# Optimization experiments

Measured on AMD Instinct MI355X. Metric: run time of the kernel, lower is better.

## Reference

```python
import jax, jax.numpy as jnp
import numpy as np

B, C, H, W = 8, 256, 56, 56
K = 3  # kernel size


def _unfold3x3(x):
    """torch nn.Unfold(kernel=3, stride=1, pad=1) -> [B, HW, C*9].

    torch orders the unfolded channel dim as (c, ki, kj) with c slowest.
    """
    b, c, h, w = x.shape
    xp = jnp.pad(x, ((0, 0), (0, 0), (1, 1), (1, 1)))
    # stack 9 shifted views -> [B, C, 9, H, W]
    patches = jnp.stack(
        [xp[:, :, i:i + h, j:j + w] for i in range(K) for j in range(K)],
        axis=2,
    )
    return patches.reshape(b, c * K * K, h * w).transpose(0, 2, 1)


def setup_inputs() -> dict:
    key = jax.random.key(0)
    ks = jax.random.split(key, 8)
    d = C * K * K  # 2304
    s1 = 1.0 / np.sqrt(d)
    s2 = 1.0 / np.sqrt(C)
    return {
        "x": jax.random.normal(ks[0], (B, C, H, W), jnp.float32),
        "W1": jax.random.uniform(ks[1], (d, C), jnp.float32, -s1, s1),
        "b1": jax.random.uniform(ks[2], (C,), jnp.float32, -s1, s1),
        "W2": jax.random.uniform(ks[3], (C, d), jnp.float32, -s2, s2),
        "b2": jax.random.uniform(ks[4], (d,), jnp.float32, -s2, s2),
        "W3": jax.random.uniform(ks[5], (d, C), jnp.float32, -s1, s1),
        "b3": jax.random.uniform(ks[6], (C,), jnp.float32, -s1, s1),
    }


def reference(x, W1, b1, W2, b2, W3, b3):
    t = _unfold3x3(x)                                   # [B, HW, C*9]
    h1 = jax.nn.relu(jnp.einsum('bld,dc->blc', t, W1) + b1)   # [B, HW, C]
    s = jax.nn.sigmoid(jnp.einsum('blc,cd->bld', h1, W2) + b2)  # [B, HW, C*9]
    out = jnp.einsum('bld,dc->blc', t * s, W3) + b3     # [B, HW, C]
    return out
```

## Files before the change

kernel.cpp:

```cpp
#include <hip/hip_runtime.h>

typedef unsigned short u16;
typedef unsigned int u32;
typedef __attribute__((ext_vector_type(8))) short bfrag_t;
typedef __attribute__((ext_vector_type(4))) float accfrag_t;

__device__ __forceinline__ u16 f2b(float f) {
    u32 u = __float_as_uint(f);
    u32 r = (u + 0x7FFFu + ((u >> 16) & 1u)) >> 16;
    return (u16)r;
}
__device__ __forceinline__ float b2f(u16 b) {
    return __uint_as_float(((u32)b) << 16);
}

__device__ __forceinline__ void load16(const u16* g, u16* l) {
    __builtin_amdgcn_global_load_lds(
        (__attribute__((address_space(1))) void*)(u16*)g,
        (__attribute__((address_space(3))) void*)l,
        16, 0, 0);
}

__global__ __launch_bounds__(256) void k_xtp(const float* __restrict__ x,
                                             u16* __restrict__ xtp) {
    const int bh = blockIdx.x;
    const int b = bh / 58;
    const int hp = bh - b * 58;
    const int tid = threadIdx.x;
    u16* rowbase = xtp + (size_t)(b * 58 + hp) * 58 * 256;
    if (hp == 0 || hp == 57) {
        u32* p = (u32*)rowbase;
        for (int i = tid; i < 58 * 128; i += 256) p[i] = 0;
        return;
    }
    __shared__ float lds[256 * 57];
    const int h = hp - 1;
    const float* xb = x + (size_t)b * 802816 + h * 56;
    for (int idx = tid; idx < 256 * 56; idx += 256) {
        int c = idx / 56;
        int w = idx - c * 56;
        lds[c * 57 + w] = xb[c * 3136 + w];
    }
    __syncthreads();
    rowbase[tid] = 0;
    rowbase[57 * 256 + tid] = 0;
    for (int wp = 1; wp <= 56; ++wp)
        rowbase[wp * 256 + tid] = f2b(lds[tid * 57 + (wp - 1)]);
}

__global__ __launch_bounds__(256) void k_wprep(
    const float* __restrict__ W1, const float* __restrict__ W2,
    const float* __restrict__ W3, const float* __restrict__ b2,
    u16* __restrict__ W1f, u16* __restrict__ W2f,
    u16* __restrict__ W3f, float* __restrict__ b2p) {
    const int bid = blockIdx.x;
    const int tid = threadIdx.x;
    if (bid < 144) {
        const float* in = bid < 72 ? W1 : W3;
        u16* out = bid < 72 ? W1f : W3f;
        const int b = bid < 72 ? bid : bid - 72;
        const int rrp = b >> 3;
        const int cg = b & 7;
        __shared__ u16 lds1[8192];
        for (int cc = 0; cc < 32; ++cc) {
            int d = (cg * 32 + cc) * 9 + rrp;
            lds1[cc * 256 + tid] = f2b(in[d * 256 + tid]);
        }
        __syncthreads();
        const int kc72 = rrp * 8 + cg;
        const int w = tid >> 5;
        const int j = (tid >> 4) & 1;
        u16* ob = out + (w * 72 + kc72) * 1024 + ((tid * 32) & 1023);
        for (int s = 0; s < 32; ++s) {
            int o = tid * 32 + s;
            int e = o & 7, ln = (o >> 3) & 63;
            int n = w * 32 + j * 16 + (ln & 15);
            int q = (ln >> 4) * 8 + e;
            ob[s] = lds1[q * 256 + n];
        }
    } else if (bid < 216) {
        const int b = bid - 144;
        const int rr = b >> 3;
        const int w = b & 7;
        __shared__ u16 lds2[8192];
        for (int s = 0; s < 32; ++s) {
            int li = s * 256 + tid;
            int k = li >> 5, dloc = li & 31;
            lds2[k * 32 + dloc] = f2b(W2[k * 2304 + (w * 32 + dloc) * 9 + rr]);
        }
        __syncthreads();
        u16* ob = W2f + (rr * 8 + w) * 8192 + tid * 32;
        for (int s = 0; s < 32; ++s) {
            int o = tid * 32 + s;
            int e = o & 7, ln = (o >> 3) & 63, j = (o >> 9) & 1, kc = o >> 10;
            int k = kc * 32 + (ln >> 4) * 8 + e;
            int dloc = j * 16 + (ln & 15);
            ob[s] = lds2[k * 32 + dloc];
        }
    } else {
        int idx = (bid - 216) * 256 + tid;
        if (idx < 2304) b2p[idx] = b2[(idx & 255) * 9 + (idx >> 8)];
    }
}

__global__ __launch_bounds__(512, 4) void k_fused(
    const u16* __restrict__ xtp, const u16* __restrict__ W1f,
    const u16* __restrict__ W2f, const u16* __restrict__ W3f,
    const float* __restrict__ b1, const float* __restrict__ b2p,
    const float* __restrict__ b3, float* __restrict__ out) {
    __shared__ __align__(16) u16 As[16384];
    __shared__ __align__(16) u16 Us[16384];

    const int tid = threadIdx.x;
    const int wave = tid >> 6;
    const int lane = tid & 63;
    const int fr = lane & 15;
    const int fq = lane >> 4;
    const int l0 = blockIdx.x * 64;

    const int srow = (tid >> 2) & 63;
    const int hi = tid >> 8;
    int roff;
    {
        int l = l0 + srow;
        int b = l / 3136;
        int rem = l - b * 3136;
        int h = rem / 56;
        int w = rem - h * 56;
        roff = ((b * 58 + h + 1) * 58 + (w + 1)) * 256 + (tid & 3) * 8;
    }
    u16* ldsStage = As + (wave & 3) * 512 + lane * 8;

    accfrag_t acc[4][2], accO[4][2];
#pragma unroll
    for (int i = 0; i < 4; ++i)
#pragma unroll
        for (int j = 0; j < 2; ++j) {
            acc[i][j] = (accfrag_t)0.f;
            accO[i][j] = (accfrag_t)0.f;
        }

    const u16* w1p = W1f + wave * 73728 + lane * 8;
    for (int rr = 0; rr < 9; ++rr) {
        const int shift = ((rr / 3 - 1) * 58 + (rr % 3) - 1) * 256;
        __syncthreads();
#pragma unroll
        for (int q = 0; q < 4; ++q) {
            const int kc = 2 * q + hi;
            load16(xtp + roff + shift + kc * 32, ldsStage + kc * 2048);
        }
        __syncthreads();
#pragma unroll
        for (int kc = 0; kc < 8; ++kc) {
            bfrag_t bf[2], af[4];
#pragma unroll
            for (int j = 0; j < 2; ++j)
                bf[j] = *(const bfrag_t*)(w1p + ((rr * 8 + kc) * 2 + j) * 512);
#pragma unroll
            for (int i = 0; i < 4; ++i)
                af[i] = *(const bfrag_t*)(As + kc * 2048 + (i * 16 + fr) * 32 + fq * 8);
#pragma unroll
            for (int i = 0; i < 4; ++i)
#pragma unroll
                for (int j = 0; j < 2; ++j)
                    acc[i][j] = __builtin_amdgcn_mfma_f32_16x16x32_bf16(
                        af[i], bf[j], acc[i][j], 0, 0, 0);
        }
    }
    __syncthreads();
#pragma unroll
    for (int i = 0; i < 4; ++i) {
#pragma unroll
        for (int j = 0; j < 2; ++j) {
            const int col = wave * 32 + j * 16 + fr;
            const float bv = b1[col];
#pragma unroll
            for (int r = 0; r < 4; ++r) {
                float v = acc[i][j][r] + bv;
                v = v > 0.f ? v : 0.f;
                const float vh = __shfl_down(v, 1);
                if (!(lane & 1)) {
                    u32 pk = (u32)f2b(v) | ((u32)f2b(vh) << 16);
                    *(u32*)&As[wave * 2048 + (i * 16 + fq * 4 + r) * 32 + j * 16 + fr] = pk;
                }
            }
        }
    }
    __syncthreads();

    const u16* w3p = W3f + wave * 73728 + lane * 8;
    for (int rr = 0; rr < 9; ++rr) {
        const int shift = ((rr / 3 - 1) * 58 + (rr % 3) - 1) * 256;
#pragma unroll
        for (int i = 0; i < 4; ++i)
#pragma unroll
            for (int j = 0; j < 2; ++j) acc[i][j] = (accfrag_t)0.f;
        const u16* w2p = W2f + (rr * 8 + wave) * 8192 + lane * 8;
#pragma unroll
        for (int kc = 0; kc < 8; ++kc) {
            bfrag_t bf[2], af[4];
#pragma unroll
            for (int j = 0; j < 2; ++j)
                bf[j] = *(const bfrag_t*)(w2p + (kc * 2 + j) * 512);
#pragma unroll
            for (int i = 0; i < 4; ++i)
                af[i] = *(const bfrag_t*)(As + kc * 2048 + (i * 16 + fr) * 32 + fq * 8);
#pragma unroll
            for (int i = 0; i < 4; ++i)
#pragma unroll
                for (int j = 0; j < 2; ++j)
                    acc[i][j] = __builtin_amdgcn_mfma_f32_16x16x32_bf16(
                        af[i], bf[j], acc[i][j], 0, 0, 0);
        }
        __syncthreads();
#pragma unroll
        for (int i = 0; i < 4; ++i) {
#pragma unroll
            for (int j = 0; j < 2; ++j) {
                const int colh = wave * 32 + j * 16 + fr;
                const float bv = b2p[rr * 256 + colh];
#pragma unroll
                for (int r = 0; r < 4; ++r) {
                    const float z = acc[i][j][r] + bv;
                    const float s = 1.f / (1.f + __expf(-z));
                    const float sh = __shfl_down(s, 1);
                    if (!(lane & 1)) {
                        u32 pk = (u32)f2b(s) | ((u32)f2b(sh) << 16);
                        *(u32*)&Us[wave * 2048 + (i * 16 + fq * 4 + r) * 32 + j * 16 + fr] = pk;
                    }
                }
            }
        }
        __syncthreads();
#pragma unroll
        for (int q = 0; q < 4; ++q) {
            const int kc = 2 * q + hi;
            const int idx = kc * 2048 + ((tid * 8) & 2047);
            bfrag_t sv = *(const bfrag_t*)(Us + idx);
            bfrag_t tv = *(const bfrag_t*)(xtp + roff + shift + kc * 32);
            bfrag_t rv;
#pragma unroll
            for (int e = 0; e < 8; ++e)
                rv[e] = (short)f2b(b2f((u16)sv[e]) * b2f((u16)tv[e]));
            *(bfrag_t*)(Us + idx) = rv;
        }
        __syncthreads();
#pragma unroll
        for (int kc = 0; kc < 8; ++kc) {
            bfrag_t bf[2], af[4];
#pragma unroll
            for (int j = 0; j < 2; ++j)
                bf[j] = *(const bfrag_t*)(w3p + ((rr * 8 + kc) * 2 + j) * 512);
#pragma unroll
            for (int i = 0; i < 4; ++i)
                af[i] = *(const bfrag_t*)(Us + kc * 2048 + (i * 16 + fr) * 32 + fq * 8);
#pragma unroll
            for (int i = 0; i < 4; ++i)
#pragma unroll
                for (int j = 0; j < 2; ++j)
                    accO[i][j] = __builtin_amdgcn_mfma_f32_16x16x32_bf16(
                        af[i], bf[j], accO[i][j], 0, 0, 0);
        }
    }

#pragma unroll
    for (int i = 0; i < 4; ++i) {
#pragma unroll
        for (int j = 0; j < 2; ++j) {
            const int col = wave * 32 + j * 16 + fr;
            const float bv = b3[col];
#pragma unroll
            for (int r = 0; r < 4; ++r) {
                const float v = accO[i][j][r] + bv;
                const float vh = __shfl_down(v, 1);
                if (!(lane & 1)) {
                    float2 st = make_float2(v, vh);
                    *(float2*)(out + (size_t)(l0 + i * 16 + fq * 4 + r) * 256 + col) = st;
                }
            }
        }
    }
}

extern "C" void kernel_launch(void* const* d_in, const int* in_sizes, int n_in,
                              void* d_out, int out_size, void* d_ws, size_t ws_size,
                              hipStream_t stream) {
    const float* x  = (const float*)d_in[0];
    const float* W1 = (const float*)d_in[1];
    const float* b1 = (const float*)d_in[2];
    const float* W2 = (const float*)d_in[3];
    const float* b2 = (const float*)d_in[4];
    const float* W3 = (const float*)d_in[5];
    const float* b3 = (const float*)d_in[6];
    float* out = (float*)d_out;

    char* ws = (char*)d_ws;
    u16* xtp = (u16*)ws;  ws += (size_t)8 * 58 * 58 * 256 * 2;
    u16* W1f = (u16*)ws;  ws += (size_t)589824 * 2;
    u16* W2f = (u16*)ws;  ws += (size_t)589824 * 2;
    u16* W3f = (u16*)ws;  ws += (size_t)589824 * 2;
    float* b2p = (float*)ws;

    k_wprep<<<225, 256, 0, stream>>>(W1, W2, W3, b2, W1f, W2f, W3f, b2p);
    k_xtp<<<464, 256, 0, stream>>>(x, xtp);
    k_fused<<<392, 512, 0, stream>>>(xtp, W1f, W2f, W3f, b1, b2p, b3, out);
}
```

Measured before the change: 229.8 us.

## Merge prep kernels, double-buffer unfold staging, prefetch patches, use packed bf16 converts

Folds the x-transpose and weight-prep kernels into one launch and rewrites the weight shuffles so consecutive threads write consecutive outputs. The first GEMM now double-buffers its patch staging between the two LDS buffers, loading the next shift while the current one is computed. This removes one barrier per step. Phase three prefetches the patch vectors into registers before the W2 GEMM and uses the hardware packed bf16 convert and an approximate reciprocal in the sigmoid. The packed convert and rcp may round slightly differently from the software paths they replace.

Result: faster. 205.9 us (-10.4%).

```diff
diff --git a/kernel.cpp b/kernel.cpp
--- a/kernel.cpp
+++ b/kernel.cpp
@@ -4,15 +4,20 @@
 typedef unsigned int u32;
 typedef __attribute__((ext_vector_type(8))) short bfrag_t;
 typedef __attribute__((ext_vector_type(4))) float accfrag_t;
+typedef __attribute__((ext_vector_type(4))) u32 u32x4;
 
 __device__ __forceinline__ u16 f2b(float f) {
     u32 u = __float_as_uint(f);
     u32 r = (u + 0x7FFFu + ((u >> 16) & 1u)) >> 16;
     return (u16)r;
 }
-__device__ __forceinline__ float b2f(u16 b) {
-    return __uint_as_float(((u32)b) << 16);
-}
+__device__ __forceinline__ u32 pkbf16(float lo, float hi) {
+    u32 r;
+    asm("v_cvt_pk_bf16_f32 %0, %1, %2" : "=v"(r) : "v"(lo), "v"(hi));
+    return r;
+}
+__device__ __forceinline__ float blo(u32 v) { return __uint_as_float(v << 16); }
+__device__ __forceinline__ float bhi(u32 v) { return __uint_as_float(v & 0xffff0000u); }
 
 __device__ __forceinline__ void load16(const u16* g, u16* l) {
     __builtin_amdgcn_global_load_lds(
@@ -21,84 +26,85 @@
         16, 0, 0);
 }
 
-__global__ __launch_bounds__(256) void k_xtp(const float* __restrict__ x,
-                                             u16* __restrict__ xtp) {
-    const int bh = blockIdx.x;
-    const int b = bh / 58;
-    const int hp = bh - b * 58;
-    const int tid = threadIdx.x;
-    u16* rowbase = xtp + (size_t)(b * 58 + hp) * 58 * 256;
-    if (hp == 0 || hp == 57) {
-        u32* p = (u32*)rowbase;
-        for (int i = tid; i < 58 * 128; i += 256) p[i] = 0;
-        return;
-    }
-    __shared__ float lds[256 * 57];
-    const int h = hp - 1;
-    const float* xb = x + (size_t)b * 802816 + h * 56;
-    for (int idx = tid; idx < 256 * 56; idx += 256) {
-        int c = idx / 56;
-        int w = idx - c * 56;
-        lds[c * 57 + w] = xb[c * 3136 + w];
-    }
-    __syncthreads();
-    rowbase[tid] = 0;
-    rowbase[57 * 256 + tid] = 0;
-    for (int wp = 1; wp <= 56; ++wp)
-        rowbase[wp * 256 + tid] = f2b(lds[tid * 57 + (wp - 1)]);
-}
-
-__global__ __launch_bounds__(256) void k_wprep(
-    const float* __restrict__ W1, const float* __restrict__ W2,
-    const float* __restrict__ W3, const float* __restrict__ b2,
+__global__ __launch_bounds__(256) void k_prep(
+    const float* __restrict__ x, const float* __restrict__ W1,
+    const float* __restrict__ W2, const float* __restrict__ W3,
+    const float* __restrict__ b2, u16* __restrict__ xtp,
     u16* __restrict__ W1f, u16* __restrict__ W2f,
     u16* __restrict__ W3f, float* __restrict__ b2p) {
+    __shared__ __align__(16) char smem[58368];
     const int bid = blockIdx.x;
     const int tid = threadIdx.x;
-    if (bid < 144) {
-        const float* in = bid < 72 ? W1 : W3;
-        u16* out = bid < 72 ? W1f : W3f;
-        const int b = bid < 72 ? bid : bid - 72;
+    if (bid < 464) {
+        const int b = bid / 58;
+        const int hp = bid - b * 58;
+        u16* rowbase = xtp + (size_t)(b * 58 + hp) * 58 * 256;
+        if (hp == 0 || hp == 57) {
+            u32* p = (u32*)rowbase;
+            for (int i = tid; i < 58 * 128; i += 256) p[i] = 0;
+            return;
+        }
+        float* lds = (float*)smem;
+        const int h = hp - 1;
+        const float* xb = x + (size_t)b * 802816 + h * 56;
+        for (int idx = tid; idx < 256 * 56; idx += 256) {
+            int c = idx / 56;
+            int w = idx - c * 56;
+            lds[c * 57 + w] = xb[c * 3136 + w];
+        }
+        __syncthreads();
+        rowbase[tid] = 0;
+        rowbase[57 * 256 + tid] = 0;
+        for (int wp = 1; wp <= 56; ++wp)
+            rowbase[wp * 256 + tid] = f2b(lds[tid * 57 + (wp - 1)]);
+    } else if (bid < 608) {
+        int b = bid - 464;
+        const float* in = b < 72 ? W1 : W3;
+        u16* out = b < 72 ? W1f : W3f;
+        if (b >= 72) b -= 72;
         const int rrp = b >> 3;
         const int cg = b & 7;
-        __shared__ u16 lds1[8192];
+        u16* lds1 = (u16*)smem;
         for (int cc = 0; cc < 32; ++cc) {
             int d = (cg * 32 + cc) * 9 + rrp;
             lds1[cc * 256 + tid] = f2b(in[d * 256 + tid]);
         }
         __syncthreads();
         const int kc72 = rrp * 8 + cg;
-        const int w = tid >> 5;
-        const int j = (tid >> 4) & 1;
-        u16* ob = out + (w * 72 + kc72) * 1024 + ((tid * 32) & 1023);
         for (int s = 0; s < 32; ++s) {
-            int o = tid * 32 + s;
-            int e = o & 7, ln = (o >> 3) & 63;
-            int n = w * 32 + j * 16 + (ln & 15);
-            int q = (ln >> 4) * 8 + e;
-            ob[s] = lds1[q * 256 + n];
-        }
-    } else if (bid < 216) {
-        const int b = bid - 144;
+            const int w = s >> 2;
+            const int o = (s & 3) * 256 + tid;
+            const int e = o & 7;
+            const int ln = (o >> 3) & 63;
+            const int j = o >> 9;
+            const int n = w * 32 + j * 16 + (ln & 15);
+            const int q = (ln >> 4) * 8 + e;
+            out[(w * 72 + kc72) * 1024 + o] = lds1[q * 256 + n];
+        }
+    } else if (bid < 680) {
+        const int b = bid - 608;
         const int rr = b >> 3;
         const int w = b & 7;
-        __shared__ u16 lds2[8192];
+        u16* lds2 = (u16*)smem;
         for (int s = 0; s < 32; ++s) {
             int li = s * 256 + tid;
             int k = li >> 5, dloc = li & 31;
             lds2[k * 32 + dloc] = f2b(W2[k * 2304 + (w * 32 + dloc) * 9 + rr]);
         }
         __syncthreads();
-        u16* ob = W2f + (rr * 8 + w) * 8192 + tid * 32;
+        u16* ob = W2f + (rr * 8 + w) * 8192;
         for (int s = 0; s < 32; ++s) {
-            int o = tid * 32 + s;
-            int e = o & 7, ln = (o >> 3) & 63, j = (o >> 9) & 1, kc = o >> 10;
-            int k = kc * 32 + (ln >> 4) * 8 + e;
-            int dloc = j * 16 + (ln & 15);
-            ob[s] = lds2[k * 32 + dloc];
+            const int o = s * 256 + tid;
+            const int e = o & 7;
+            const int ln = (o >> 3) & 63;
+            const int j = (o >> 9) & 1;
+            const int kc = o >> 10;
+            const int k = kc * 32 + (ln >> 4) * 8 + e;
+            const int dloc = j * 16 + (ln & 15);
+            ob[o] = lds2[k * 32 + dloc];
         }
     } else {
-        int idx = (bid - 216) * 256 + tid;
+        int idx = (bid - 680) * 256 + tid;
         if (idx < 2304) b2p[idx] = b2[(idx & 255) * 9 + (idx >> 8)];
     }
 }
@@ -117,19 +123,26 @@
     const int fr = lane & 15;
     const int fq = lane >> 4;
     const int l0 = blockIdx.x * 64;
-
-    const int srow = (tid >> 2) & 63;
     const int hi = tid >> 8;
+
     int roff;
     {
-        int l = l0 + srow;
+        int l = l0 + ((tid >> 2) & 63);
         int b = l / 3136;
         int rem = l - b * 3136;
         int h = rem / 56;
         int w = rem - h * 56;
         roff = ((b * 58 + h + 1) * 58 + (w + 1)) * 256 + (tid & 3) * 8;
     }
-    u16* ldsStage = As + (wave & 3) * 512 + lane * 8;
+    const int stageOff = (wave & 3) * 512 + lane * 8;
+    auto shiftOf = [](int rr) { return ((rr / 3 - 1) * 58 + (rr % 3) - 1) * 256; };
+    auto stage = [&](u16* buf, int shift) {
+#pragma unroll
+        for (int q = 0; q < 4; ++q) {
+            const int kc = 2 * q + hi;
+            load16(xtp + roff + shift + kc * 32, buf + kc * 2048 + stageOff);
+        }
+    };
 
     accfrag_t acc[4][2], accO[4][2];
 #pragma unroll
@@ -141,15 +154,12 @@
         }
 
     const u16* w1p = W1f + wave * 73728 + lane * 8;
+    stage(As, shiftOf(0));
     for (int rr = 0; rr < 9; ++rr) {
-        const int shift = ((rr / 3 - 1) * 58 + (rr % 3) - 1) * 256;
-        __syncthreads();
-#pragma unroll
-        for (int q = 0; q < 4; ++q) {
-            const int kc = 2 * q + hi;
-            load16(xtp + roff + shift + kc * 32, ldsStage + kc * 2048);
-        }
-        __syncthreads();
+        u16* cur = (rr & 1) ? Us : As;
+        u16* nxt = (rr & 1) ? As : Us;
+        __syncthreads();
+        if (rr < 8) stage(nxt, shiftOf(rr + 1));
 #pragma unroll
         for (int kc = 0; kc < 8; ++kc) {
             bfrag_t bf[2], af[4];
@@ -158,7 +168,7 @@
                 bf[j] = *(const bfrag_t*)(w1p + ((rr * 8 + kc) * 2 + j) * 512);
 #pragma unroll
             for (int i = 0; i < 4; ++i)
-                af[i] = *(const bfrag_t*)(As + kc * 2048 + (i * 16 + fr) * 32 + fq * 8);
+                af[i] = *(const bfrag_t*)(cur + kc * 2048 + (i * 16 + fr) * 32 + fq * 8);
 #pragma unroll
             for (int i = 0; i < 4; ++i)
 #pragma unroll
@@ -172,17 +182,15 @@
     for (int i = 0; i < 4; ++i) {
 #pragma unroll
         for (int j = 0; j < 2; ++j) {
-            const int col = wave * 32 + j * 16 + fr;
-            const float bv = b1[col];
+            const float bv = b1[wave * 32 + j * 16 + fr];
 #pragma unroll
             for (int r = 0; r < 4; ++r) {
                 float v = acc[i][j][r] + bv;
                 v = v > 0.f ? v : 0.f;
                 const float vh = __shfl_down(v, 1);
-                if (!(lane & 1)) {
-                    u32 pk = (u32)f2b(v) | ((u32)f2b(vh) << 16);
-                    *(u32*)&As[wave * 2048 + (i * 16 + fq * 4 + r) * 32 + j * 16 + fr] = pk;
-                }
+                if (!(lane & 1))
+                    *(u32*)&As[wave * 2048 + (i * 16 + fq * 4 + r) * 32 + j * 16 + fr] =
+                        pkbf16(v, vh);
             }
         }
     }
@@ -190,7 +198,13 @@
 
     const u16* w3p = W3f + wave * 73728 + lane * 8;
     for (int rr = 0; rr < 9; ++rr) {
-        const int shift = ((rr / 3 - 1) * 58 + (rr % 3) - 1) * 256;
+        const int shift = shiftOf(rr);
+        u32x4 tvreg[4];
+#pragma unroll
+        for (int q = 0; q < 4; ++q) {
+            const int kc = 2 * q + hi;
+            tvreg[q] = *(const u32x4*)(xtp + roff + shift + kc * 32);
+        }
 #pragma unroll
         for (int i = 0; i < 4; ++i)
 #pragma unroll
@@ -217,17 +231,15 @@
         for (int i = 0; i < 4; ++i) {
 #pragma unroll
             for (int j = 0; j < 2; ++j) {
-                const int colh = wave * 32 + j * 16 + fr;
-                const float bv = b2p[rr * 256 + colh];
+                const float bv = b2p[rr * 256 + wave * 32 + j * 16 + fr];
 #pragma unroll
                 for (int r = 0; r < 4; ++r) {
                     const float z = acc[i][j][r] + bv;
-                    const float s = 1.f / (1.f + __expf(-z));
+                    const float s = __builtin_amdgcn_rcpf(1.f + __expf(-z));
                     const float sh = __shfl_down(s, 1);
-                    if (!(lane & 1)) {
-                        u32 pk = (u32)f2b(s) | ((u32)f2b(sh) << 16);
-                        *(u32*)&Us[wave * 2048 + (i * 16 + fq * 4 + r) * 32 + j * 16 + fr] = pk;
-                    }
+                    if (!(lane & 1))
+                        *(u32*)&Us[wave * 2048 + (i * 16 + fq * 4 + r) * 32 + j * 16 + fr] =
+                            pkbf16(s, sh);
                 }
             }
         }
@@ -236,13 +248,13 @@
         for (int q = 0; q < 4; ++q) {
             const int kc = 2 * q + hi;
             const int idx = kc * 2048 + ((tid * 8) & 2047);
-            bfrag_t sv = *(const bfrag_t*)(Us + idx);
-            bfrag_t tv = *(const bfrag_t*)(xtp + roff + shift + kc * 32);
-            bfrag_t rv;
-#pragma unroll
-            for (int e = 0; e < 8; ++e)
-                rv[e] = (short)f2b(b2f((u16)sv[e]) * b2f((u16)tv[e]));
-            *(bfrag_t*)(Us + idx) = rv;
+            u32x4 sv = *(const u32x4*)(Us + idx);
+            u32x4 rv;
+#pragma unroll
+            for (int e = 0; e < 4; ++e)
+                rv[e] = pkbf16(blo(sv[e]) * blo(tvreg[q][e]),
+                               bhi(sv[e]) * bhi(tvreg[q][e]));
+            *(u32x4*)(Us + idx) = rv;
         }
         __syncthreads();
 #pragma unroll
@@ -301,7 +313,6 @@
     u16* W3f = (u16*)ws;  ws += (size_t)589824 * 2;
     float* b2p = (float*)ws;
 
-    k_wprep<<<225, 256, 0, stream>>>(W1, W2, W3, b2, W1f, W2f, W3f, b2p);
-    k_xtp<<<464, 256, 0, stream>>>(x, xtp);
+    k_prep<<<689, 256, 0, stream>>>(x, W1, W2, W3, b2, xtp, W1f, W2f, W3f, b2p);
     k_fused<<<392, 512, 0, stream>>>(xtp, W1f, W2f, W3f, b1, b2p, b3, out);
 }
```
